# Performance work log

Measured on AMD Instinct MI355X. Metric: run time of the kernel, lower is better.

## Reference

```python
import jax, jax.numpy as jnp
import numpy as np

N_EMBD = 1024
N_HEAD = 16
HEAD_DIM = N_EMBD // N_HEAD


def setup_inputs() -> dict:
    key = jax.random.key(0)
    ks = jax.random.split(key, 9)
    B, T, C = 4, 2048, N_EMBD
    s = 1.0 / np.sqrt(C)
    return {
        "x": jax.random.normal(ks[0], (B, T, C), dtype=jnp.float32),
        "Wq": jax.random.normal(ks[1], (C, C), dtype=jnp.float32) * s,
        "bq": jnp.zeros((C,), dtype=jnp.float32),
        "Wk": jax.random.normal(ks[2], (C, C), dtype=jnp.float32) * s,
        "bk": jnp.zeros((C,), dtype=jnp.float32),
        "Wv": jax.random.normal(ks[3], (C, C), dtype=jnp.float32) * s,
        "bv": jnp.zeros((C,), dtype=jnp.float32),
        "Wo": jax.random.normal(ks[4], (C, C), dtype=jnp.float32) * s,
        "bo": jnp.zeros((C,), dtype=jnp.float32),
    }


def reference(x, Wq, bq, Wk, bk, Wv, bv, Wo, bo):
    B, T, C = x.shape
    H, D = N_HEAD, HEAD_DIM
    # torch Linear: y = x @ W.T + b ; here W stored as (in, out) so y = x @ W + b
    q = (x @ Wq + bq).reshape(B, T, H, D).transpose(0, 2, 1, 3)  # [B,H,T,D]
    k = (x @ Wk + bk).reshape(B, T, H, D).transpose(0, 2, 1, 3)
    v = (x @ Wv + bv).reshape(B, T, H, D).transpose(0, 2, 1, 3)
    scores = jnp.einsum('bhqd,bhkd->bhqk', q, k) / jnp.sqrt(jnp.float32(D))
    causal = jnp.tril(jnp.ones((T, T), dtype=bool))  # [T,T]
    scores = jnp.where(causal[None, None, :, :], scores, -jnp.inf)
    weights = jax.nn.softmax(scores, axis=-1)
    # dropout disabled (eval mode / deterministic reference)
    out = jnp.einsum('bhqk,bhkd->bhqd', weights, v)  # [B,H,T,D]
    out = out.transpose(0, 2, 1, 3).reshape(B, T, C)
    return out @ Wo + bo
```

## Files before the change

### kernel.cpp

```cpp
#include <hip/hip_runtime.h>
#include <stdint.h>
#include <stddef.h>

#define NB 4
#define NT 2048
#define NC 1024
#define NH 16
#define ND 64
#define NM (NB*NT)

typedef __bf16 bf16_t;
typedef __attribute__((ext_vector_type(8)))  __bf16 bf16x8;
typedef __attribute__((ext_vector_type(4)))  __bf16 bf16x4;
typedef __attribute__((ext_vector_type(2)))  __bf16 bf16x2;
typedef __attribute__((ext_vector_type(4)))  float  f32x4;
typedef __attribute__((ext_vector_type(16))) float  f32x16;
typedef __attribute__((ext_vector_type(4)))  unsigned int u32x4;

#define QK_SCALE_LOG2E 0.18033688011112042f

__device__ __forceinline__ f32x4 mfma_bf16(bf16x8 a, bf16x8 b, f32x4 c) {
  return __builtin_amdgcn_mfma_f32_16x16x32_bf16(a, b, c, 0, 0, 0);
}
__device__ __forceinline__ f32x16 mfma32(bf16x8 a, bf16x8 b, f32x16 c) {
  return __builtin_amdgcn_mfma_f32_32x32x16_bf16(a, b, c, 0, 0, 0);
}

__device__ __forceinline__ void gld_lds16(const void* g, void* l) {
  __builtin_amdgcn_global_load_lds(
      (const __attribute__((address_space(1))) void*)g,
      (__attribute__((address_space(3))) void*)l, 16, 0, 0);
}

__device__ __forceinline__ unsigned int pack_bf16(float a, float b) {
  bf16x2 t; t[0] = (bf16_t)a; t[1] = (bf16_t)b;
  return __builtin_bit_cast(unsigned int, t);
}

#if __has_builtin(__builtin_amdgcn_permlane32_swap)
typedef __attribute__((ext_vector_type(2))) unsigned int u32x2;
__device__ __forceinline__ void plswap(unsigned int &a, unsigned int &b) {
  u32x2 r = __builtin_amdgcn_permlane32_swap(a, b, false, false);
  a = r[0]; b = r[1];
}
#else
__device__ __forceinline__ void plswap(unsigned int &a, unsigned int &b) {
  asm volatile("s_nop 1\n\tv_permlane32_swap_b32 %0, %1\n\ts_nop 1"
               : "+v"(a), "+v"(b));
}
#endif

__global__ __launch_bounds__(256) void prep_kernel(
    const float* __restrict__ x, const float* __restrict__ Wq,
    const float* __restrict__ Wk, const float* __restrict__ Wv,
    const float* __restrict__ Wo,
    bf16_t* __restrict__ xb, bf16_t* __restrict__ Tq, bf16_t* __restrict__ Tk,
    bf16_t* __restrict__ Tv, bf16_t* __restrict__ To) {
  __shared__ float tile[32][33];
  if (blockIdx.x < 4096) {
    const int wsel = blockIdx.x >> 10;
    const float* W = (wsel == 0) ? Wq : (wsel == 1) ? Wk : (wsel == 2) ? Wv : Wo;
    bf16_t*     WT = (wsel == 0) ? Tq : (wsel == 1) ? Tk : (wsel == 2) ? Tv : To;
    const int blk = blockIdx.x & 1023;
    const int t = threadIdx.x;
    const int tx = t & 31, ty = t >> 5;
    const int k0 = (blk & 31) << 5;
    const int n0 = (blk >> 5) << 5;
#pragma unroll
    for (int i = 0; i < 4; ++i)
      tile[ty + 8*i][tx] = W[(size_t)(k0 + ty + 8*i)*NC + n0 + tx];
    __syncthreads();
#pragma unroll
    for (int i = 0; i < 4; ++i)
      WT[(size_t)(n0 + ty + 8*i)*NC + k0 + tx] = (bf16_t)tile[tx][ty + 8*i];
  } else {
    const int n4 = NM*NC/4;
    const int stride = 2048 * 256;
    for (int i = (blockIdx.x - 4096) * 256 + threadIdx.x; i < n4; i += stride) {
      float4 v = reinterpret_cast<const float4*>(x)[i];
      bf16x4 o;
      o[0] = (bf16_t)v.x; o[1] = (bf16_t)v.y; o[2] = (bf16_t)v.z; o[3] = (bf16_t)v.w;
      reinterpret_cast<bf16x4*>(xb)[i] = o;
    }
  }
}

template<int MODE>
__global__ __launch_bounds__(512, 2) void gemm_bt256_kernel(
    const bf16_t* __restrict__ A, const bf16_t* __restrict__ BT,
    int M, int N, int K,
    bf16_t* __restrict__ qo, bf16_t* __restrict__ ko, bf16_t* __restrict__ vo,
    const float* __restrict__ b0, const float* __restrict__ b1, const float* __restrict__ b2,
    float* __restrict__ outp, const float* __restrict__ bo)
{
  const int tid  = threadIdx.x;
  const int lane = tid & 63;
  const int wv   = tid >> 6;
  const int wr   = wv >> 1, wc = wv & 1;
  const int l15  = lane & 15, lg = lane >> 4;

  const int nbn = N >> 7;
  const int cpx = gridDim.x >> 3;
  const int swz = (blockIdx.x & 7)*cpx + (blockIdx.x >> 3);
  const int bm = swz / nbn, bn = swz % nbn;
  const int m0 = bm << 8, n0 = bn << 7;

  __shared__ char smem[98304];

  f32x4 acc[4][4] = {};

  int offa[4], offb[2];
#pragma unroll
  for (int p = 0; p < 4; ++p) {
    const int c = p*512 + tid;
    const int row = c >> 3, ch = (c & 7) ^ (row & 7);
    offa[p] = row*K + (ch << 3);
  }
#pragma unroll
  for (int p = 0; p < 2; ++p) {
    const int c = p*512 + tid;
    const int row = c >> 3, ch = (c & 7) ^ (row & 7);
    offb[p] = row*K + (ch << 3);
  }
  const int sega = wv << 10;

  const bf16_t* Ab = A  + (size_t)m0 * K;
  const bf16_t* Bb = BT + (size_t)n0 * K;

  const int nkt = K >> 6;

  {
    char* const As = smem;
    char* const Bs = smem + 32768;
#pragma unroll
    for (int p = 0; p < 4; ++p) gld_lds16(Ab + offa[p], As + p*8192 + sega);
#pragma unroll
    for (int p = 0; p < 2; ++p) gld_lds16(Bb + offb[p], Bs + p*8192 + sega);
  }

  for (int kt = 0; kt < nkt; ++kt) {
    char* const As = smem + (kt & 1)*49152;
    char* const Bs = As + 32768;

    asm volatile("s_waitcnt vmcnt(0)" ::: "memory");
    __builtin_amdgcn_s_barrier();
    __builtin_amdgcn_sched_barrier(0);

    if (kt + 1 < nkt) {
      char* const An = smem + ((kt + 1) & 1)*49152;
      char* const Bn = An + 32768;
      const int k0 = (kt + 1) << 6;
#pragma unroll
      for (int p = 0; p < 4; ++p) gld_lds16(Ab + k0 + offa[p], An + p*8192 + sega);
#pragma unroll
      for (int p = 0; p < 2; ++p) gld_lds16(Bb + k0 + offb[p], Bn + p*8192 + sega);
      __builtin_amdgcn_sched_barrier(0);
    }

#pragma unroll
    for (int ks = 0; ks < 2; ++ks) {
      bf16x8 af[4], bfr[4];
#pragma unroll
      for (int fr = 0; fr < 4; ++fr) {
        const int row = wr*64 + fr*16 + l15;
        const int ch  = (ks*4 + lg) ^ (row & 7);
        af[fr] = *reinterpret_cast<const bf16x8*>(As + row*128 + ch*16);
      }
#pragma unroll
      for (int fc = 0; fc < 4; ++fc) {
        const int row = wc*64 + fc*16 + l15;
        const int ch  = (ks*4 + lg) ^ (row & 7);
        bfr[fc] = *reinterpret_cast<const bf16x8*>(Bs + row*128 + ch*16);
      }
      __builtin_amdgcn_s_setprio(1);
#pragma unroll
      for (int fr = 0; fr < 4; ++fr)
#pragma unroll
        for (int fc = 0; fc < 4; ++fc)
          acc[fr][fc] = mfma_bf16(af[fr], bfr[fc], acc[fr][fc]);
      __builtin_amdgcn_s_setprio(0);
    }
  }

  if (MODE == 0 && n0 >= 2*NC) {
    bf16_t* vbuf = (bf16_t*)smem;
    const int VSTR = 264;
    __syncthreads();
#pragma unroll
    for (int fr = 0; fr < 4; ++fr) {
#pragma unroll
      for (int fc = 0; fc < 4; ++fc) {
        const int zl = wc*64 + fc*16 + l15;
        const int tl = wr*64 + fr*16 + (lg << 2);
        const float bias = b2[(n0 - 2*NC) + zl];
        bf16x4 ov;
#pragma unroll
        for (int r = 0; r < 4; ++r) ov[r] = (bf16_t)(acc[fr][fc][r] + bias);
        *reinterpret_cast<bf16x4*>(&vbuf[zl*VSTR + tl]) = ov;
      }
    }
    __syncthreads();
    const int zl  = tid >> 2;
    const int t0l = (tid & 3) << 6;
    const int zg  = (n0 - 2*NC) + zl;
    const int h   = zg >> 6, d = zg & 63;
    const int bbv = m0 >> 11;
    bf16_t* dst = vo + ((((size_t)bbv*NH + h)*ND + d)*NT) + (m0 & (NT-1)) + t0l;
#pragma unroll
    for (int u = 0; u < 8; ++u)
      *reinterpret_cast<bf16x8*>(dst + u*8) =
          *reinterpret_cast<const bf16x8*>(&vbuf[zl*VSTR + t0l + u*8]);
  } else {
#pragma unroll
    for (int fr = 0; fr < 4; ++fr) {
#pragma unroll
      for (int fc = 0; fc < 4; ++fc) {
        const int mrow0 = m0 + wr*64 + fr*16 + (lg << 2);
        const int ncol  = n0 + wc*64 + fc*16 + l15;
        if (MODE == 0) {
          const int mat = ncol >> 10, c = ncol & 1023;
          const int h = c >> 6, d = c & 63;
          bf16_t* dst = (mat == 0) ? qo : ko;
          const float* bptr = (mat == 0) ? b0 : b1;
          const float bias = bptr[c];
          const float scl = (mat == 0) ? QK_SCALE_LOG2E : 1.0f;
#pragma unroll
          for (int r = 0; r < 4; ++r) {
            const int mm = mrow0 + r;
            const int bb = mm >> 11, tt = mm & (NT - 1);
            dst[((((size_t)bb*NH + h)*NT + tt) << 6) + d] =
                (bf16_t)((acc[fr][fc][r] + bias) * scl);
          }
        } else {
          const float bias = bo[ncol];
#pragma unroll
          for (int r = 0; r < 4; ++r)
            outp[(size_t)(mrow0 + r)*N + ncol] = acc[fr][fc][r] + bias;
        }
      }
    }
  }
}

__global__ __launch_bounds__(256, 2) void attn_kernel(
    const bf16_t* __restrict__ q, const bf16_t* __restrict__ k, const bf16_t* __restrict__ vt,
    bf16_t* __restrict__ o)
{
  const int tid  = threadIdx.x;
  const int lane = tid & 63;
  const int wv   = tid >> 6;
  const int l31  = lane & 31, h = lane >> 5;

  const int tpair = blockIdx.x >> 6;
  const int bh    = blockIdx.x & 63;
  const int bb = bh >> 4, hh = bh & 15;

  __shared__ char smem[65536];
  char* const ks0 = smem;
  char* const ks1 = smem + 16384;
  char* const vs0 = smem + 32768;
  char* const vs1 = smem + 49152;

  const size_t base = (size_t)bh * (NT * ND);
  const bf16_t* Kg = k  + base;
  const bf16_t* Vg = vt + base;

  int offk[4], offv[4], segb[4];
#pragma unroll
  for (int p = 0; p < 4; ++p) {
    const int c = p*256 + tid;
    const int krow = c >> 3;
    const int kch  = (c & 7) ^ (krow & 7);
    offk[p] = krow*ND + (kch << 3);
    const int vrow = c >> 4;
    const int vdc  = (c & 15) ^ (vrow & 15);
    offv[p] = vrow*NT + (vdc << 3);
    segb[p] = (p*4 + wv) << 10;
  }

  bf16x8 ones8;
#pragma unroll
  for (int i = 0; i < 8; ++i) ones8[i] = (bf16_t)1.0f;

#pragma unroll
  for (int p = 0; p < 4; ++p) {
    gld_lds16(Kg + offk[p], ks0 + segb[p]);
    gld_lds16(Vg + offv[p], vs0 + segb[p]);
  }

  int jj = 0;

#pragma unroll 1
  for (int pass = 0; pass < 2; ++pass) {
    const int tile = (pass == 0) ? tpair : 15 - tpair;
    const int q0   = tile << 7;
    const int q0w  = q0 + wv*32;
    const int qg   = q0w + l31;

    bf16x8 qf[4];
    {
      const bf16_t* Qg = q + base + (size_t)qg*ND + 8*h;
#pragma unroll
      for (int ds = 0; ds < 4; ++ds)
        qf[ds] = *reinterpret_cast<const bf16x8*>(Qg + 16*ds);
    }

    f32x16 oc[2] = {};
    f32x16 lacc = {};

    const int nkv = tile + 1;

#pragma unroll 1
    for (int j = 0; j < nkv; ++j, ++jj) {
      const bool cur1 = (jj & 1) != 0;
      char* const Kc = cur1 ? ks1 : ks0;
      char* const Vc = cur1 ? vs1 : vs0;

      asm volatile("s_waitcnt vmcnt(0)" ::: "memory");
      __builtin_amdgcn_s_barrier();
      __builtin_amdgcn_sched_barrier(0);

      int nj = (j + 1 < nkv) ? (j + 1) : ((pass == 0) ? 0 : -1);
      if (nj >= 0) {
        char* const Kn = cur1 ? ks0 : ks1;
        char* const Vn = cur1 ? vs0 : vs1;
        const bf16_t* kp = Kg + (size_t)nj*(128*ND);
        const bf16_t* vp = Vg + (size_t)nj*128;
#pragma unroll
        for (int p = 0; p < 4; ++p) {
          gld_lds16(kp + offk[p], Kn + segb[p]);
          gld_lds16(vp + offv[p], Vn + segb[p]);
        }
        __builtin_amdgcn_sched_barrier(0);
      }

      const int ktile0 = j << 7;
      const int kb1 = ktile0 + 64;
      const bool h1 = (kb1 <= q0w + 31);

      if (h1) {
        f32x16 st0[2] = {}, st1[2] = {};

        __builtin_amdgcn_s_setprio(1);
#pragma unroll
        for (int ds = 0; ds < 4; ++ds) {
#pragma unroll
          for (int kt = 0; kt < 2; ++kt) {
            const int r0 = kt*32 + l31;
            const int c0 = (2*ds + h) ^ (r0 & 7);
            const bf16x8 k0 = *reinterpret_cast<const bf16x8*>(Kc + r0*128 + c0*16);
            st0[kt] = mfma32(k0, qf[ds], st0[kt]);
            const int r1 = (2 + kt)*32 + l31;
            const int c1 = (2*ds + h) ^ (r1 & 7);
            const bf16x8 k1 = *reinterpret_cast<const bf16x8*>(Kc + r1*128 + c1*16);
            st1[kt] = mfma32(k1, qf[ds], st1[kt]);
          }
        }
        __builtin_amdgcn_s_setprio(0);
        __builtin_amdgcn_sched_barrier(0);

        if (ktile0 + 63 > q0w) {
          const int qrel = qg - ktile0 - 4*h;
#pragma unroll
          for (int kt = 0; kt < 2; ++kt)
#pragma unroll
            for (int r = 0; r < 16; ++r) {
              const int kc = (r & 3) + 8*(r >> 2) + 32*kt;
              st0[kt][r] = (kc > qrel) ? 0.0f : exp2f(st0[kt][r]);
            }
        } else {
#pragma unroll
          for (int kt = 0; kt < 2; ++kt)
#pragma unroll
            for (int r = 0; r < 16; ++r)
              st0[kt][r] = exp2f(st0[kt][r]);
        }
        if (kb1 + 63 > q0w) {
          const int qrel = qg - kb1 - 4*h;
#pragma unroll
          for (int kt = 0; kt < 2; ++kt)
#pragma unroll
            for (int r = 0; r < 16; ++r) {
              const int kc = (r & 3) + 8*(r >> 2) + 32*kt;
              st1[kt][r] = (kc > qrel) ? 0.0f : exp2f(st1[kt][r]);
            }
        } else {
#pragma unroll
          for (int kt = 0; kt < 2; ++kt)
#pragma unroll
            for (int r = 0; r < 16; ++r)
              st1[kt][r] = exp2f(st1[kt][r]);
        }
        __builtin_amdgcn_sched_barrier(0);

#pragma unroll
        for (int kt = 0; kt < 2; ++kt) {
#pragma unroll
          for (int g = 0; g < 2; ++g) {
            {
              unsigned int wa = pack_bf16(st0[kt][8*g + 0], st0[kt][8*g + 1]);
              unsigned int wb = pack_bf16(st0[kt][8*g + 2], st0[kt][8*g + 3]);
              unsigned int wc = pack_bf16(st0[kt][8*g + 4], st0[kt][8*g + 5]);
              unsigned int wd = pack_bf16(st0[kt][8*g + 6], st0[kt][8*g + 7]);
              plswap(wa, wc); plswap(wb, wd);
              u32x4 pb; pb[0] = wa; pb[1] = wb; pb[2] = wc; pb[3] = wd;
              const bf16x8 pf = __builtin_bit_cast(bf16x8, pb);
              const int cv = 2*(2*kt + g) + h;
              __builtin_amdgcn_s_setprio(1);
              lacc = mfma32(ones8, pf, lacc);
#pragma unroll
              for (int da = 0; da < 2; ++da) {
                const int row = 32*da + l31;
                const int lcv = cv ^ (row & 15);
                const bf16x8 vf = *reinterpret_cast<const bf16x8*>(Vc + row*256 + lcv*16);
                oc[da] = mfma32(vf, pf, oc[da]);
              }
              __builtin_amdgcn_s_setprio(0);
            }
            {
              unsigned int wa = pack_bf16(st1[kt][8*g + 0], st1[kt][8*g + 1]);
              unsigned int wb = pack_bf16(st1[kt][8*g + 2], st1[kt][8*g + 3]);
              unsigned int wc = pack_bf16(st1[kt][8*g + 4], st1[kt][8*g + 5]);
              unsigned int wd = pack_bf16(st1[kt][8*g + 6], st1[kt][8*g + 7]);
              plswap(wa, wc); plswap(wb, wd);
              u32x4 pb; pb[0] = wa; pb[1] = wb; pb[2] = wc; pb[3] = wd;
              const bf16x8 pf = __builtin_bit_cast(bf16x8, pb);
              const int cv = 2*(4 + 2*kt + g) + h;
              __builtin_amdgcn_s_setprio(1);
              lacc = mfma32(ones8, pf, lacc);
#pragma unroll
              for (int da = 0; da < 2; ++da) {
                const int row = 32*da + l31;
                const int lcv = cv ^ (row & 15);
                const bf16x8 vf = *reinterpret_cast<const bf16x8*>(Vc + row*256 + lcv*16);
                oc[da] = mfma32(vf, pf, oc[da]);
              }
              __builtin_amdgcn_s_setprio(0);
            }
          }
        }
      } else {
        f32x16 st[2] = {};
        __builtin_amdgcn_s_setprio(1);
#pragma unroll
        for (int ds = 0; ds < 4; ++ds) {
#pragma unroll
          for (int kt = 0; kt < 2; ++kt) {
            const int row = kt*32 + l31;
            const int cl  = (2*ds + h) ^ (row & 7);
            const bf16x8 kfr = *reinterpret_cast<const bf16x8*>(Kc + row*128 + cl*16);
            st[kt] = mfma32(kfr, qf[ds], st[kt]);
          }
        }
        __builtin_amdgcn_s_setprio(0);

        if (ktile0 + 63 > q0w) {
          const int qrel = qg - ktile0 - 4*h;
#pragma unroll
          for (int kt = 0; kt < 2; ++kt)
#pragma unroll
            for (int r = 0; r < 16; ++r) {
              const int kc = (r & 3) + 8*(r >> 2) + 32*kt;
              st[kt][r] = (kc > qrel) ? 0.0f : exp2f(st[kt][r]);
            }
        } else {
#pragma unroll
          for (int kt = 0; kt < 2; ++kt)
#pragma unroll
            for (int r = 0; r < 16; ++r)
              st[kt][r] = exp2f(st[kt][r]);
        }

#pragma unroll
        for (int kt = 0; kt < 2; ++kt) {
#pragma unroll
          for (int g = 0; g < 2; ++g) {
            unsigned int wa = pack_bf16(st[kt][8*g + 0], st[kt][8*g + 1]);
            unsigned int wb = pack_bf16(st[kt][8*g + 2], st[kt][8*g + 3]);
            unsigned int wc = pack_bf16(st[kt][8*g + 4], st[kt][8*g + 5]);
            unsigned int wd = pack_bf16(st[kt][8*g + 6], st[kt][8*g + 7]);
            plswap(wa, wc); plswap(wb, wd);
            u32x4 pb; pb[0] = wa; pb[1] = wb; pb[2] = wc; pb[3] = wd;
            const bf16x8 pf = __builtin_bit_cast(bf16x8, pb);
            const int cv = 2*(2*kt + g) + h;
            __builtin_amdgcn_s_setprio(1);
            lacc = mfma32(ones8, pf, lacc);
#pragma unroll
            for (int da = 0; da < 2; ++da) {
              const int row = 32*da + l31;
              const int lcv = cv ^ (row & 15);
              const bf16x8 vf = *reinterpret_cast<const bf16x8*>(Vc + row*256 + lcv*16);
              oc[da] = mfma32(vf, pf, oc[da]);
            }
            __builtin_amdgcn_s_setprio(0);
          }
        }
      }
    }

    const float rl = 1.0f / lacc[0];
    bf16_t* orow = o + ((size_t)bb*NT + qg)*NC + hh*ND;
#pragma unroll
    for (int da = 0; da < 2; ++da) {
#pragma unroll
      for (int u = 0; u < 4; ++u) {
        bf16x4 ov;
#pragma unroll
        for (int i = 0; i < 4; ++i) ov[i] = (bf16_t)(oc[da][4*u + i] * rl);
        *reinterpret_cast<bf16x4*>(orow + 32*da + 8*u + 4*h) = ov;
      }
    }
  }
}

extern "C" void kernel_launch(void* const* d_in, const int* in_sizes, int n_in,
                              void* d_out, int out_size, void* d_ws, size_t ws_size,
                              hipStream_t stream) {
  (void)in_sizes; (void)n_in; (void)out_size;
  const float* x  = (const float*)d_in[0];
  const float* Wq = (const float*)d_in[1];
  const float* bq = (const float*)d_in[2];
  const float* Wk = (const float*)d_in[3];
  const float* bk = (const float*)d_in[4];
  const float* Wv = (const float*)d_in[5];
  const float* bv = (const float*)d_in[6];
  const float* Wo = (const float*)d_in[7];
  const float* bo = (const float*)d_in[8];
  float* out = (float*)d_out;

  const size_t off_xb    = 0;
  const size_t off_wqkvT = 16777216;
  const size_t off_woT   = 23068672;
  const size_t off_q     = 25165824;
  const size_t off_k     = 41943040;
  const size_t off_v     = 58720256;
  const size_t off_attn  = 75497472;
  const size_t need      = 92274688;
  if (ws_size < need) return;

  char* ws = (char*)d_ws;
  bf16_t* xb    = (bf16_t*)(ws + off_xb);
  bf16_t* wqkvT = (bf16_t*)(ws + off_wqkvT);
  bf16_t* woT   = (bf16_t*)(ws + off_woT);
  bf16_t* qb    = (bf16_t*)(ws + off_q);
  bf16_t* kb    = (bf16_t*)(ws + off_k);
  bf16_t* vtb   = (bf16_t*)(ws + off_v);
  bf16_t* attnb = (bf16_t*)(ws + off_attn);

  prep_kernel<<<dim3(6144), dim3(256), 0, stream>>>(
      x, Wq, Wk, Wv, Wo, xb, wqkvT, wqkvT + 1048576, wqkvT + 2097152, woT);

  gemm_bt256_kernel<0><<<dim3(768), dim3(512), 0, stream>>>(
      xb, wqkvT, NM, 3*NC, NC, qb, kb, vtb, bq, bk, bv, nullptr, nullptr);

  attn_kernel<<<dim3(8*64), dim3(256), 0, stream>>>(qb, kb, vtb, attnb);

  gemm_bt256_kernel<1><<<dim3(256), dim3(512), 0, stream>>>(
      attnb, woT, NM, NC, NC, nullptr, nullptr, nullptr, nullptr, nullptr, nullptr,
      out, bo);
}
```

Measured before the change: 160.9 us.

## Restructure attention blocks to 8-wave 256-query tiles instead of paired 128-query passes

The attention kernel now launches 512-thread blocks that each handle one 256-row query tile, with eight waves sharing K/V tiles loaded into LDS. This replaces the earlier design, where each 4-wave block ran two passes over complementary 128-row tiles to balance causal work. Each K/V tile load is now reused across twice as many query rows, which cuts global-to-LDS traffic and removes the pass loop. In exchange, the lower waves in a block skip masked KV tiles and sit idle while still joining the barriers. Load balance now comes from interleaving heavy and light tiles across blockIdx halves, and the launch bounds request higher occupancy.

```diff
diff --git a/kernel.cpp b/kernel.cpp
--- a/kernel.cpp
+++ b/kernel.cpp
@@ -242,7 +242,7 @@
   }
 }
 
-__global__ __launch_bounds__(256, 2) void attn_kernel(
+__global__ __launch_bounds__(512, 4) void attn_kernel(
     const bf16_t* __restrict__ q, const bf16_t* __restrict__ k, const bf16_t* __restrict__ vt,
     bf16_t* __restrict__ o)
 {
@@ -251,9 +251,13 @@
   const int wv   = tid >> 6;
   const int l31  = lane & 31, h = lane >> 5;
 
-  const int tpair = blockIdx.x >> 6;
-  const int bh    = blockIdx.x & 63;
+  const int slot = blockIdx.x & 255;
+  const int s    = blockIdx.x >> 8;
+  const int bh   = slot & 63;
+  const int tg   = slot >> 6;
+  const int st   = s ? (7 - tg) : tg;
   const int bb = bh >> 4, hh = bh & 15;
+  const int q0 = st << 8;
 
   __shared__ char smem[65536];
   char* const ks0 = smem;
@@ -265,17 +269,20 @@
   const bf16_t* Kg = k  + base;
   const bf16_t* Vg = vt + base;
 
-  int offk[4], offv[4], segb[4];
-#pragma unroll
-  for (int p = 0; p < 4; ++p) {
-    const int c = p*256 + tid;
+  const int q0w = q0 + wv*32;
+  const int qg  = q0w + l31;
+
+  int offk[2], offv[2], segb[2];
+#pragma unroll
+  for (int p = 0; p < 2; ++p) {
+    const int c = p*512 + tid;
     const int krow = c >> 3;
     const int kch  = (c & 7) ^ (krow & 7);
     offk[p] = krow*ND + (kch << 3);
     const int vrow = c >> 4;
     const int vdc  = (c & 15) ^ (vrow & 15);
     offv[p] = vrow*NT + (vdc << 3);
-    segb[p] = (p*4 + wv) << 10;
+    segb[p] = (p*8 + wv) << 10;
   }
 
   bf16x8 ones8;
@@ -283,202 +290,117 @@
   for (int i = 0; i < 8; ++i) ones8[i] = (bf16_t)1.0f;
 
 #pragma unroll
-  for (int p = 0; p < 4; ++p) {
+  for (int p = 0; p < 2; ++p) {
     gld_lds16(Kg + offk[p], ks0 + segb[p]);
     gld_lds16(Vg + offv[p], vs0 + segb[p]);
   }
 
-  int jj = 0;
+  bf16x8 qf[4];
+  {
+    const bf16_t* Qg = q + base + (size_t)qg*ND + 8*h;
+#pragma unroll
+    for (int ds = 0; ds < 4; ++ds)
+      qf[ds] = *reinterpret_cast<const bf16x8*>(Qg + 16*ds);
+  }
+
+  f32x16 oc[2] = {};
+  f32x16 lacc = {};
+
+  const int nkv = 2*(st + 1);
 
 #pragma unroll 1
-  for (int pass = 0; pass < 2; ++pass) {
-    const int tile = (pass == 0) ? tpair : 15 - tpair;
-    const int q0   = tile << 7;
-    const int q0w  = q0 + wv*32;
-    const int qg   = q0w + l31;
-
-    bf16x8 qf[4];
-    {
-      const bf16_t* Qg = q + base + (size_t)qg*ND + 8*h;
-#pragma unroll
-      for (int ds = 0; ds < 4; ++ds)
-        qf[ds] = *reinterpret_cast<const bf16x8*>(Qg + 16*ds);
-    }
-
-    f32x16 oc[2] = {};
-    f32x16 lacc = {};
-
-    const int nkv = tile + 1;
-
-#pragma unroll 1
-    for (int j = 0; j < nkv; ++j, ++jj) {
-      const bool cur1 = (jj & 1) != 0;
-      char* const Kc = cur1 ? ks1 : ks0;
-      char* const Vc = cur1 ? vs1 : vs0;
-
-      asm volatile("s_waitcnt vmcnt(0)" ::: "memory");
-      __builtin_amdgcn_s_barrier();
+  for (int j = 0; j < nkv; ++j) {
+    const bool cur1 = (j & 1) != 0;
+    char* const Kc = cur1 ? ks1 : ks0;
+    char* const Vc = cur1 ? vs1 : vs0;
+
+    asm volatile("s_waitcnt vmcnt(0)" ::: "memory");
+    __builtin_amdgcn_s_barrier();
+    __builtin_amdgcn_sched_barrier(0);
+
+    if (j + 1 < nkv) {
+      char* const Kn = cur1 ? ks0 : ks1;
+      char* const Vn = cur1 ? vs0 : vs1;
+      const bf16_t* kp = Kg + (size_t)(j + 1)*(128*ND);
+      const bf16_t* vp = Vg + (size_t)(j + 1)*128;
+#pragma unroll
+      for (int p = 0; p < 2; ++p) {
+        gld_lds16(kp + offk[p], Kn + segb[p]);
+        gld_lds16(vp + offv[p], Vn + segb[p]);
+      }
       __builtin_amdgcn_sched_barrier(0);
-
-      int nj = (j + 1 < nkv) ? (j + 1) : ((pass == 0) ? 0 : -1);
-      if (nj >= 0) {
-        char* const Kn = cur1 ? ks0 : ks1;
-        char* const Vn = cur1 ? vs0 : vs1;
-        const bf16_t* kp = Kg + (size_t)nj*(128*ND);
-        const bf16_t* vp = Vg + (size_t)nj*128;
-#pragma unroll
-        for (int p = 0; p < 4; ++p) {
-          gld_lds16(kp + offk[p], Kn + segb[p]);
-          gld_lds16(vp + offv[p], Vn + segb[p]);
+    }
+
+    const int ktile0 = j << 7;
+    if (ktile0 > q0w + 31) continue;
+
+    const int kb1 = ktile0 + 64;
+    const bool h1 = (kb1 <= q0w + 31);
+
+    if (h1) {
+      f32x16 st0[2] = {}, st1[2] = {};
+
+      __builtin_amdgcn_s_setprio(1);
+#pragma unroll
+      for (int ds = 0; ds < 4; ++ds) {
+#pragma unroll
+        for (int kt = 0; kt < 2; ++kt) {
+          const int r0 = kt*32 + l31;
+          const int c0 = (2*ds + h) ^ (r0 & 7);
+          const bf16x8 k0 = *reinterpret_cast<const bf16x8*>(Kc + r0*128 + c0*16);
+          st0[kt] = mfma32(k0, qf[ds], st0[kt]);
+          const int r1 = (2 + kt)*32 + l31;
+          const int c1 = (2*ds + h) ^ (r1 & 7);
+          const bf16x8 k1 = *reinterpret_cast<const bf16x8*>(Kc + r1*128 + c1*16);
+          st1[kt] = mfma32(k1, qf[ds], st1[kt]);
         }
-        __builtin_amdgcn_sched_barrier(0);
-      }
-
-      const int ktile0 = j << 7;
-      const int kb1 = ktile0 + 64;
-      const bool h1 = (kb1 <= q0w + 31);
-
-      if (h1) {
-        f32x16 st0[2] = {}, st1[2] = {};
-
-        __builtin_amdgcn_s_setprio(1);
-#pragma unroll
-        for (int ds = 0; ds < 4; ++ds) {
-#pragma unroll
-          for (int kt = 0; kt < 2; ++kt) {
-            const int r0 = kt*32 + l31;
-            const int c0 = (2*ds + h) ^ (r0 & 7);
-            const bf16x8 k0 = *reinterpret_cast<const bf16x8*>(Kc + r0*128 + c0*16);
-            st0[kt] = mfma32(k0, qf[ds], st0[kt]);
-            const int r1 = (2 + kt)*32 + l31;
-            const int c1 = (2*ds + h) ^ (r1 & 7);
-            const bf16x8 k1 = *reinterpret_cast<const bf16x8*>(Kc + r1*128 + c1*16);
-            st1[kt] = mfma32(k1, qf[ds], st1[kt]);
-          }
-        }
-        __builtin_amdgcn_s_setprio(0);
-        __builtin_amdgcn_sched_barrier(0);
-
-        if (ktile0 + 63 > q0w) {
-          const int qrel = qg - ktile0 - 4*h;
-#pragma unroll
-          for (int kt = 0; kt < 2; ++kt)
-#pragma unroll
-            for (int r = 0; r < 16; ++r) {
-              const int kc = (r & 3) + 8*(r >> 2) + 32*kt;
-              st0[kt][r] = (kc > qrel) ? 0.0f : exp2f(st0[kt][r]);
-            }
-        } else {
-#pragma unroll
-          for (int kt = 0; kt < 2; ++kt)
-#pragma unroll
-            for (int r = 0; r < 16; ++r)
-              st0[kt][r] = exp2f(st0[kt][r]);
-        }
-        if (kb1 + 63 > q0w) {
-          const int qrel = qg - kb1 - 4*h;
-#pragma unroll
-          for (int kt = 0; kt < 2; ++kt)
-#pragma unroll
-            for (int r = 0; r < 16; ++r) {
-              const int kc = (r & 3) + 8*(r >> 2) + 32*kt;
-              st1[kt][r] = (kc > qrel) ? 0.0f : exp2f(st1[kt][r]);
-            }
-        } else {
-#pragma unroll
-          for (int kt = 0; kt < 2; ++kt)
-#pragma unroll
-            for (int r = 0; r < 16; ++r)
-              st1[kt][r] = exp2f(st1[kt][r]);
-        }
-        __builtin_amdgcn_sched_barrier(0);
-
-#pragma unroll
-        for (int kt = 0; kt < 2; ++kt) {
-#pragma unroll
-          for (int g = 0; g < 2; ++g) {
-            {
-              unsigned int wa = pack_bf16(st0[kt][8*g + 0], st0[kt][8*g + 1]);
-              unsigned int wb = pack_bf16(st0[kt][8*g + 2], st0[kt][8*g + 3]);
-              unsigned int wc = pack_bf16(st0[kt][8*g + 4], st0[kt][8*g + 5]);
-              unsigned int wd = pack_bf16(st0[kt][8*g + 6], st0[kt][8*g + 7]);
-              plswap(wa, wc); plswap(wb, wd);
-              u32x4 pb; pb[0] = wa; pb[1] = wb; pb[2] = wc; pb[3] = wd;
-              const bf16x8 pf = __builtin_bit_cast(bf16x8, pb);
-              const int cv = 2*(2*kt + g) + h;
-              __builtin_amdgcn_s_setprio(1);
-              lacc = mfma32(ones8, pf, lacc);
-#pragma unroll
-              for (int da = 0; da < 2; ++da) {
-                const int row = 32*da + l31;
-                const int lcv = cv ^ (row & 15);
-                const bf16x8 vf = *reinterpret_cast<const bf16x8*>(Vc + row*256 + lcv*16);
-                oc[da] = mfma32(vf, pf, oc[da]);
-              }
-              __builtin_amdgcn_s_setprio(0);
-            }
-            {
-              unsigned int wa = pack_bf16(st1[kt][8*g + 0], st1[kt][8*g + 1]);
-              unsigned int wb = pack_bf16(st1[kt][8*g + 2], st1[kt][8*g + 3]);
-              unsigned int wc = pack_bf16(st1[kt][8*g + 4], st1[kt][8*g + 5]);
-              unsigned int wd = pack_bf16(st1[kt][8*g + 6], st1[kt][8*g + 7]);
-              plswap(wa, wc); plswap(wb, wd);
-              u32x4 pb; pb[0] = wa; pb[1] = wb; pb[2] = wc; pb[3] = wd;
-              const bf16x8 pf = __builtin_bit_cast(bf16x8, pb);
-              const int cv = 2*(4 + 2*kt + g) + h;
-              __builtin_amdgcn_s_setprio(1);
-              lacc = mfma32(ones8, pf, lacc);
-#pragma unroll
-              for (int da = 0; da < 2; ++da) {
-                const int row = 32*da + l31;
-                const int lcv = cv ^ (row & 15);
-                const bf16x8 vf = *reinterpret_cast<const bf16x8*>(Vc + row*256 + lcv*16);
-                oc[da] = mfma32(vf, pf, oc[da]);
-              }
-              __builtin_amdgcn_s_setprio(0);
-            }
-          }
-        }
+      }
+      __builtin_amdgcn_s_setprio(0);
+      __builtin_amdgcn_sched_barrier(0);
+
+      if (ktile0 + 63 > q0w) {
+        const int qrel = qg - ktile0 - 4*h;
+#pragma unroll
+        for (int kt = 0; kt < 2; ++kt)
+#pragma unroll
+          for (int r = 0; r < 16; ++r) {
+            const int kc = (r & 3) + 8*(r >> 2) + 32*kt;
+            st0[kt][r] = (kc > qrel) ? 0.0f : exp2f(st0[kt][r]);
+          }
       } else {
-        f32x16 st[2] = {};
-        __builtin_amdgcn_s_setprio(1);
-#pragma unroll
-        for (int ds = 0; ds < 4; ++ds) {
-#pragma unroll
-          for (int kt = 0; kt < 2; ++kt) {
-            const int row = kt*32 + l31;
-            const int cl  = (2*ds + h) ^ (row & 7);
-            const bf16x8 kfr = *reinterpret_cast<const bf16x8*>(Kc + row*128 + cl*16);
-            st[kt] = mfma32(kfr, qf[ds], st[kt]);
-          }
-        }
-        __builtin_amdgcn_s_setprio(0);
-
-        if (ktile0 + 63 > q0w) {
-          const int qrel = qg - ktile0 - 4*h;
-#pragma unroll
-          for (int kt = 0; kt < 2; ++kt)
-#pragma unroll
-            for (int r = 0; r < 16; ++r) {
-              const int kc = (r & 3) + 8*(r >> 2) + 32*kt;
-              st[kt][r] = (kc > qrel) ? 0.0f : exp2f(st[kt][r]);
-            }
-        } else {
-#pragma unroll
-          for (int kt = 0; kt < 2; ++kt)
-#pragma unroll
-            for (int r = 0; r < 16; ++r)
-              st[kt][r] = exp2f(st[kt][r]);
-        }
-
-#pragma unroll
-        for (int kt = 0; kt < 2; ++kt) {
-#pragma unroll
-          for (int g = 0; g < 2; ++g) {
-            unsigned int wa = pack_bf16(st[kt][8*g + 0], st[kt][8*g + 1]);
-            unsigned int wb = pack_bf16(st[kt][8*g + 2], st[kt][8*g + 3]);
-            unsigned int wc = pack_bf16(st[kt][8*g + 4], st[kt][8*g + 5]);
-            unsigned int wd = pack_bf16(st[kt][8*g + 6], st[kt][8*g + 7]);
+#pragma unroll
+        for (int kt = 0; kt < 2; ++kt)
+#pragma unroll
+          for (int r = 0; r < 16; ++r)
+            st0[kt][r] = exp2f(st0[kt][r]);
+      }
+      if (kb1 + 63 > q0w) {
+        const int qrel = qg - kb1 - 4*h;
+#pragma unroll
+        for (int kt = 0; kt < 2; ++kt)
+#pragma unroll
+          for (int r = 0; r < 16; ++r) {
+            const int kc = (r & 3) + 8*(r >> 2) + 32*kt;
+            st1[kt][r] = (kc > qrel) ? 0.0f : exp2f(st1[kt][r]);
+          }
+      } else {
+#pragma unroll
+        for (int kt = 0; kt < 2; ++kt)
+#pragma unroll
+          for (int r = 0; r < 16; ++r)
+            st1[kt][r] = exp2f(st1[kt][r]);
+      }
+      __builtin_amdgcn_sched_barrier(0);
+
+#pragma unroll
+      for (int kt = 0; kt < 2; ++kt) {
+#pragma unroll
+        for (int g = 0; g < 2; ++g) {
+          {
+            unsigned int wa = pack_bf16(st0[kt][8*g + 0], st0[kt][8*g + 1]);
+            unsigned int wb = pack_bf16(st0[kt][8*g + 2], st0[kt][8*g + 3]);
+            unsigned int wc = pack_bf16(st0[kt][8*g + 4], st0[kt][8*g + 5]);
+            unsigned int wd = pack_bf16(st0[kt][8*g + 6], st0[kt][8*g + 7]);
             plswap(wa, wc); plswap(wb, wd);
             u32x4 pb; pb[0] = wa; pb[1] = wb; pb[2] = wc; pb[3] = wd;
             const bf16x8 pf = __builtin_bit_cast(bf16x8, pb);
@@ -494,21 +416,97 @@
             }
             __builtin_amdgcn_s_setprio(0);
           }
+          {
+            unsigned int wa = pack_bf16(st1[kt][8*g + 0], st1[kt][8*g + 1]);
+            unsigned int wb = pack_bf16(st1[kt][8*g + 2], st1[kt][8*g + 3]);
+            unsigned int wc = pack_bf16(st1[kt][8*g + 4], st1[kt][8*g + 5]);
+            unsigned int wd = pack_bf16(st1[kt][8*g + 6], st1[kt][8*g + 7]);
+            plswap(wa, wc); plswap(wb, wd);
+            u32x4 pb; pb[0] = wa; pb[1] = wb; pb[2] = wc; pb[3] = wd;
+            const bf16x8 pf = __builtin_bit_cast(bf16x8, pb);
+            const int cv = 2*(4 + 2*kt + g) + h;
+            __builtin_amdgcn_s_setprio(1);
+            lacc = mfma32(ones8, pf, lacc);
+#pragma unroll
+            for (int da = 0; da < 2; ++da) {
+              const int row = 32*da + l31;
+              const int lcv = cv ^ (row & 15);
+              const bf16x8 vf = *reinterpret_cast<const bf16x8*>(Vc + row*256 + lcv*16);
+              oc[da] = mfma32(vf, pf, oc[da]);
+            }
+            __builtin_amdgcn_s_setprio(0);
+          }
         }
       }
-    }
-
-    const float rl = 1.0f / lacc[0];
-    bf16_t* orow = o + ((size_t)bb*NT + qg)*NC + hh*ND;
-#pragma unroll
-    for (int da = 0; da < 2; ++da) {
-#pragma unroll
-      for (int u = 0; u < 4; ++u) {
-        bf16x4 ov;
-#pragma unroll
-        for (int i = 0; i < 4; ++i) ov[i] = (bf16_t)(oc[da][4*u + i] * rl);
-        *reinterpret_cast<bf16x4*>(orow + 32*da + 8*u + 4*h) = ov;
-      }
+    } else {
+      f32x16 st[2] = {};
+      __builtin_amdgcn_s_setprio(1);
+#pragma unroll
+      for (int ds = 0; ds < 4; ++ds) {
+#pragma unroll
+        for (int kt = 0; kt < 2; ++kt) {
+          const int row = kt*32 + l31;
+          const int cl  = (2*ds + h) ^ (row & 7);
+          const bf16x8 kfr = *reinterpret_cast<const bf16x8*>(Kc + row*128 + cl*16);
+          st[kt] = mfma32(kfr, qf[ds], st[kt]);
+        }
+      }
+      __builtin_amdgcn_s_setprio(0);
+
+      if (ktile0 + 63 > q0w) {
+        const int qrel = qg - ktile0 - 4*h;
+#pragma unroll
+        for (int kt = 0; kt < 2; ++kt)
+#pragma unroll
+          for (int r = 0; r < 16; ++r) {
+            const int kc = (r & 3) + 8*(r >> 2) + 32*kt;
+            st[kt][r] = (kc > qrel) ? 0.0f : exp2f(st[kt][r]);
+          }
+      } else {
+#pragma unroll
+        for (int kt = 0; kt < 2; ++kt)
+#pragma unroll
+          for (int r = 0; r < 16; ++r)
+            st[kt][r] = exp2f(st[kt][r]);
+      }
+
+#pragma unroll
+      for (int kt = 0; kt < 2; ++kt) {
+#pragma unroll
+        for (int g = 0; g < 2; ++g) {
+          unsigned int wa = pack_bf16(st[kt][8*g + 0], st[kt][8*g + 1]);
+          unsigned int wb = pack_bf16(st[kt][8*g + 2], st[kt][8*g + 3]);
+          unsigned int wc = pack_bf16(st[kt][8*g + 4], st[kt][8*g + 5]);
+          unsigned int wd = pack_bf16(st[kt][8*g + 6], st[kt][8*g + 7]);
+          plswap(wa, wc); plswap(wb, wd);
+          u32x4 pb; pb[0] = wa; pb[1] = wb; pb[2] = wc; pb[3] = wd;
+          const bf16x8 pf = __builtin_bit_cast(bf16x8, pb);
+          const int cv = 2*(2*kt + g) + h;
+          __builtin_amdgcn_s_setprio(1);
+          lacc = mfma32(ones8, pf, lacc);
+#pragma unroll
+          for (int da = 0; da < 2; ++da) {
+            const int row = 32*da + l31;
+            const int lcv = cv ^ (row & 15);
+            const bf16x8 vf = *reinterpret_cast<const bf16x8*>(Vc + row*256 + lcv*16);
+            oc[da] = mfma32(vf, pf, oc[da]);
+          }
+          __builtin_amdgcn_s_setprio(0);
+        }
+      }
+    }
+  }
+
+  const float rl = 1.0f / lacc[0];
+  bf16_t* orow = o + ((size_t)bb*NT + qg)*NC + hh*ND;
+#pragma unroll
+  for (int da = 0; da < 2; ++da) {
+#pragma unroll
+    for (int u = 0; u < 4; ++u) {
+      bf16x4 ov;
+#pragma unroll
+      for (int i = 0; i < 4; ++i) ov[i] = (bf16_t)(oc[da][4*u + i] * rl);
+      *reinterpret_cast<bf16x4*>(orow + 32*da + 8*u + 4*h) = ov;
     }
   }
 }
@@ -553,7 +551,7 @@
   gemm_bt256_kernel<0><<<dim3(768), dim3(512), 0, stream>>>(
       xb, wqkvT, NM, 3*NC, NC, qb, kb, vtb, bq, bk, bv, nullptr, nullptr);
 
-  attn_kernel<<<dim3(8*64), dim3(256), 0, stream>>>(qb, kb, vtb, attnb);
+  attn_kernel<<<dim3(512), dim3(512), 0, stream>>>(qb, kb, vtb, attnb);
 
   gemm_bt256_kernel<1><<<dim3(256), dim3(512), 0, stream>>>(
       attnb, woT, NM, NC, NC, nullptr, nullptr, nullptr, nullptr, nullptr, nullptr,
```

After: 329.5 us. 105% more time.

## Load K fragments directly from global into registers, drop K LDS staging

Applied to the files above, without the earlier changes.

K tiles are no longer staged through shared memory. Each lane now loads its K MFMA fragments straight from global memory into registers, and the next tile is prefetched right after the QK MFMAs. This halves LDS use to 32KB and removes the LDS reads and the swizzle arithmetic for K. The cost is 16 extra bf16x8 registers per lane, uncoalesced-ish global loads, and a vmcnt(0) wait that now also covers the K register loads. The two h1 branches are merged into a single code path.

```diff
diff --git a/kernel.cpp b/kernel.cpp
--- a/kernel.cpp
+++ b/kernel.cpp
@@ -255,23 +255,18 @@
   const int bh    = blockIdx.x & 63;
   const int bb = bh >> 4, hh = bh & 15;
 
-  __shared__ char smem[65536];
-  char* const ks0 = smem;
-  char* const ks1 = smem + 16384;
-  char* const vs0 = smem + 32768;
-  char* const vs1 = smem + 49152;
+  __shared__ char smem[32768];
+  char* const vs0 = smem;
+  char* const vs1 = smem + 16384;
 
   const size_t base = (size_t)bh * (NT * ND);
   const bf16_t* Kg = k  + base;
   const bf16_t* Vg = vt + base;
 
-  int offk[4], offv[4], segb[4];
+  int offv[4], segb[4];
 #pragma unroll
   for (int p = 0; p < 4; ++p) {
     const int c = p*256 + tid;
-    const int krow = c >> 3;
-    const int kch  = (c & 7) ^ (krow & 7);
-    offk[p] = krow*ND + (kch << 3);
     const int vrow = c >> 4;
     const int vdc  = (c & 15) ^ (vrow & 15);
     offv[p] = vrow*NT + (vdc << 3);
@@ -282,11 +277,23 @@
 #pragma unroll
   for (int i = 0; i < 8; ++i) ones8[i] = (bf16_t)1.0f;
 
-#pragma unroll
-  for (int p = 0; p < 4; ++p) {
-    gld_lds16(Kg + offk[p], ks0 + segb[p]);
+  bf16x8 kfr[4][4];
+  const bf16_t* const Kl = Kg + (size_t)l31*ND + 8*h;
+#define LOAD_K(kbase)                                                        \
+  {                                                                          \
+    const bf16_t* _kp = Kl + (size_t)(kbase)*ND;                             \
+    _Pragma("unroll")                                                        \
+    for (int _ds = 0; _ds < 4; ++_ds)                                        \
+      _Pragma("unroll")                                                      \
+      for (int _r = 0; _r < 4; ++_r)                                         \
+        kfr[_ds][_r] = *reinterpret_cast<const bf16x8*>(                     \
+            _kp + (size_t)(_r*32)*ND + 16*_ds);                              \
+  }
+
+#pragma unroll
+  for (int p = 0; p < 4; ++p)
     gld_lds16(Vg + offv[p], vs0 + segb[p]);
-  }
+  LOAD_K(0)
 
   int jj = 0;
 
@@ -313,24 +320,19 @@
 #pragma unroll 1
     for (int j = 0; j < nkv; ++j, ++jj) {
       const bool cur1 = (jj & 1) != 0;
-      char* const Kc = cur1 ? ks1 : ks0;
       char* const Vc = cur1 ? vs1 : vs0;
 
       asm volatile("s_waitcnt vmcnt(0)" ::: "memory");
       __builtin_amdgcn_s_barrier();
       __builtin_amdgcn_sched_barrier(0);
 
-      int nj = (j + 1 < nkv) ? (j + 1) : ((pass == 0) ? 0 : -1);
+      const int nj = (j + 1 < nkv) ? (j + 1) : ((pass == 0) ? 0 : -1);
       if (nj >= 0) {
-        char* const Kn = cur1 ? ks0 : ks1;
         char* const Vn = cur1 ? vs0 : vs1;
-        const bf16_t* kp = Kg + (size_t)nj*(128*ND);
         const bf16_t* vp = Vg + (size_t)nj*128;
 #pragma unroll
-        for (int p = 0; p < 4; ++p) {
-          gld_lds16(kp + offk[p], Kn + segb[p]);
+        for (int p = 0; p < 4; ++p)
           gld_lds16(vp + offv[p], Vn + segb[p]);
-        }
         __builtin_amdgcn_sched_barrier(0);
       }
 
@@ -338,43 +340,49 @@
       const int kb1 = ktile0 + 64;
       const bool h1 = (kb1 <= q0w + 31);
 
+      f32x16 st0[2] = {}, st1[2] = {};
+
+      __builtin_amdgcn_s_setprio(1);
       if (h1) {
-        f32x16 st0[2] = {}, st1[2] = {};
-
-        __builtin_amdgcn_s_setprio(1);
 #pragma unroll
         for (int ds = 0; ds < 4; ++ds) {
 #pragma unroll
           for (int kt = 0; kt < 2; ++kt) {
-            const int r0 = kt*32 + l31;
-            const int c0 = (2*ds + h) ^ (r0 & 7);
-            const bf16x8 k0 = *reinterpret_cast<const bf16x8*>(Kc + r0*128 + c0*16);
-            st0[kt] = mfma32(k0, qf[ds], st0[kt]);
-            const int r1 = (2 + kt)*32 + l31;
-            const int c1 = (2*ds + h) ^ (r1 & 7);
-            const bf16x8 k1 = *reinterpret_cast<const bf16x8*>(Kc + r1*128 + c1*16);
-            st1[kt] = mfma32(k1, qf[ds], st1[kt]);
+            st0[kt] = mfma32(kfr[ds][kt],     qf[ds], st0[kt]);
+            st1[kt] = mfma32(kfr[ds][2 + kt], qf[ds], st1[kt]);
           }
         }
-        __builtin_amdgcn_s_setprio(0);
-        __builtin_amdgcn_sched_barrier(0);
-
-        if (ktile0 + 63 > q0w) {
-          const int qrel = qg - ktile0 - 4*h;
+      } else {
+#pragma unroll
+        for (int ds = 0; ds < 4; ++ds) {
 #pragma unroll
           for (int kt = 0; kt < 2; ++kt)
-#pragma unroll
-            for (int r = 0; r < 16; ++r) {
-              const int kc = (r & 3) + 8*(r >> 2) + 32*kt;
-              st0[kt][r] = (kc > qrel) ? 0.0f : exp2f(st0[kt][r]);
-            }
-        } else {
-#pragma unroll
-          for (int kt = 0; kt < 2; ++kt)
-#pragma unroll
-            for (int r = 0; r < 16; ++r)
-              st0[kt][r] = exp2f(st0[kt][r]);
+            st0[kt] = mfma32(kfr[ds][kt], qf[ds], st0[kt]);
         }
+      }
+      __builtin_amdgcn_s_setprio(0);
+      __builtin_amdgcn_sched_barrier(0);
+
+      if (nj >= 0) { LOAD_K((size_t)nj * 128) }
+      __builtin_amdgcn_sched_barrier(0);
+
+      if (ktile0 + 63 > q0w) {
+        const int qrel = qg - ktile0 - 4*h;
+#pragma unroll
+        for (int kt = 0; kt < 2; ++kt)
+#pragma unroll
+          for (int r = 0; r < 16; ++r) {
+            const int kc = (r & 3) + 8*(r >> 2) + 32*kt;
+            st0[kt][r] = (kc > qrel) ? 0.0f : exp2f(st0[kt][r]);
+          }
+      } else {
+#pragma unroll
+        for (int kt = 0; kt < 2; ++kt)
+#pragma unroll
+          for (int r = 0; r < 16; ++r)
+            st0[kt][r] = exp2f(st0[kt][r]);
+      }
+      if (h1) {
         if (kb1 + 63 > q0w) {
           const int qrel = qg - kb1 - 4*h;
 #pragma unroll
@@ -391,98 +399,42 @@
             for (int r = 0; r < 16; ++r)
               st1[kt][r] = exp2f(st1[kt][r]);
         }
-        __builtin_amdgcn_sched_barrier(0);
-
-#pragma unroll
-        for (int kt = 0; kt < 2; ++kt) {
-#pragma unroll
-          for (int g = 0; g < 2; ++g) {
-            {
-              unsigned int wa = pack_bf16(st0[kt][8*g + 0], st0[kt][8*g + 1]);
-              unsigned int wb = pack_bf16(st0[kt][8*g + 2], st0[kt][8*g + 3]);
-              unsigned int wc = pack_bf16(st0[kt][8*g + 4], st0[kt][8*g + 5]);
-              unsigned int wd = pack_bf16(st0[kt][8*g + 6], st0[kt][8*g + 7]);
-              plswap(wa, wc); plswap(wb, wd);
-              u32x4 pb; pb[0] = wa; pb[1] = wb; pb[2] = wc; pb[3] = wd;
-              const bf16x8 pf = __builtin_bit_cast(bf16x8, pb);
-              const int cv = 2*(2*kt + g) + h;
-              __builtin_amdgcn_s_setprio(1);
-              lacc = mfma32(ones8, pf, lacc);
-#pragma unroll
-              for (int da = 0; da < 2; ++da) {
-                const int row = 32*da + l31;
-                const int lcv = cv ^ (row & 15);
-                const bf16x8 vf = *reinterpret_cast<const bf16x8*>(Vc + row*256 + lcv*16);
-                oc[da] = mfma32(vf, pf, oc[da]);
-              }
-              __builtin_amdgcn_s_setprio(0);
-            }
-            {
-              unsigned int wa = pack_bf16(st1[kt][8*g + 0], st1[kt][8*g + 1]);
-              unsigned int wb = pack_bf16(st1[kt][8*g + 2], st1[kt][8*g + 3]);
-              unsigned int wc = pack_bf16(st1[kt][8*g + 4], st1[kt][8*g + 5]);
-              unsigned int wd = pack_bf16(st1[kt][8*g + 6], st1[kt][8*g + 7]);
-              plswap(wa, wc); plswap(wb, wd);
-              u32x4 pb; pb[0] = wa; pb[1] = wb; pb[2] = wc; pb[3] = wd;
-              const bf16x8 pf = __builtin_bit_cast(bf16x8, pb);
-              const int cv = 2*(4 + 2*kt + g) + h;
-              __builtin_amdgcn_s_setprio(1);
-              lacc = mfma32(ones8, pf, lacc);
-#pragma unroll
-              for (int da = 0; da < 2; ++da) {
-                const int row = 32*da + l31;
-                const int lcv = cv ^ (row & 15);
-                const bf16x8 vf = *reinterpret_cast<const bf16x8*>(Vc + row*256 + lcv*16);
-                oc[da] = mfma32(vf, pf, oc[da]);
-              }
-              __builtin_amdgcn_s_setprio(0);
-            }
-          }
-        }
-      } else {
-        f32x16 st[2] = {};
-        __builtin_amdgcn_s_setprio(1);
-#pragma unroll
-        for (int ds = 0; ds < 4; ++ds) {
-#pragma unroll
-          for (int kt = 0; kt < 2; ++kt) {
-            const int row = kt*32 + l31;
-            const int cl  = (2*ds + h) ^ (row & 7);
-            const bf16x8 kfr = *reinterpret_cast<const bf16x8*>(Kc + row*128 + cl*16);
-            st[kt] = mfma32(kfr, qf[ds], st[kt]);
-          }
-        }
-        __builtin_amdgcn_s_setprio(0);
-
-        if (ktile0 + 63 > q0w) {
-          const int qrel = qg - ktile0 - 4*h;
-#pragma unroll
-          for (int kt = 0; kt < 2; ++kt)
-#pragma unroll
-            for (int r = 0; r < 16; ++r) {
-              const int kc = (r & 3) + 8*(r >> 2) + 32*kt;
-              st[kt][r] = (kc > qrel) ? 0.0f : exp2f(st[kt][r]);
-            }
-        } else {
-#pragma unroll
-          for (int kt = 0; kt < 2; ++kt)
-#pragma unroll
-            for (int r = 0; r < 16; ++r)
-              st[kt][r] = exp2f(st[kt][r]);
-        }
-
-#pragma unroll
-        for (int kt = 0; kt < 2; ++kt) {
-#pragma unroll
-          for (int g = 0; g < 2; ++g) {
-            unsigned int wa = pack_bf16(st[kt][8*g + 0], st[kt][8*g + 1]);
-            unsigned int wb = pack_bf16(st[kt][8*g + 2], st[kt][8*g + 3]);
-            unsigned int wc = pack_bf16(st[kt][8*g + 4], st[kt][8*g + 5]);
-            unsigned int wd = pack_bf16(st[kt][8*g + 6], st[kt][8*g + 7]);
+      }
+      __builtin_amdgcn_sched_barrier(0);
+
+#pragma unroll
+      for (int kt = 0; kt < 2; ++kt) {
+#pragma unroll
+        for (int g = 0; g < 2; ++g) {
+          {
+            unsigned int wa = pack_bf16(st0[kt][8*g + 0], st0[kt][8*g + 1]);
+            unsigned int wb = pack_bf16(st0[kt][8*g + 2], st0[kt][8*g + 3]);
+            unsigned int wc = pack_bf16(st0[kt][8*g + 4], st0[kt][8*g + 5]);
+            unsigned int wd = pack_bf16(st0[kt][8*g + 6], st0[kt][8*g + 7]);
             plswap(wa, wc); plswap(wb, wd);
             u32x4 pb; pb[0] = wa; pb[1] = wb; pb[2] = wc; pb[3] = wd;
             const bf16x8 pf = __builtin_bit_cast(bf16x8, pb);
             const int cv = 2*(2*kt + g) + h;
+            __builtin_amdgcn_s_setprio(1);
+            lacc = mfma32(ones8, pf, lacc);
+#pragma unroll
+            for (int da = 0; da < 2; ++da) {
+              const int row = 32*da + l31;
+              const int lcv = cv ^ (row & 15);
+              const bf16x8 vf = *reinterpret_cast<const bf16x8*>(Vc + row*256 + lcv*16);
+              oc[da] = mfma32(vf, pf, oc[da]);
+            }
+            __builtin_amdgcn_s_setprio(0);
+          }
+          if (h1) {
+            unsigned int wa = pack_bf16(st1[kt][8*g + 0], st1[kt][8*g + 1]);
+            unsigned int wb = pack_bf16(st1[kt][8*g + 2], st1[kt][8*g + 3]);
+            unsigned int wc = pack_bf16(st1[kt][8*g + 4], st1[kt][8*g + 5]);
+            unsigned int wd = pack_bf16(st1[kt][8*g + 6], st1[kt][8*g + 7]);
+            plswap(wa, wc); plswap(wb, wd);
+            u32x4 pb; pb[0] = wa; pb[1] = wb; pb[2] = wc; pb[3] = wd;
+            const bf16x8 pf = __builtin_bit_cast(bf16x8, pb);
+            const int cv = 2*(4 + 2*kt + g) + h;
             __builtin_amdgcn_s_setprio(1);
             lacc = mfma32(ones8, pf, lacc);
 #pragma unroll
@@ -511,6 +463,7 @@
       }
     }
   }
+#undef LOAD_K
 }
 
 extern "C" void kernel_launch(void* const* d_in, const int* in_sizes, int n_in,
```

New measurement: 186.1 us. +15.7%, slower.
